# Kernel tuning notes

Measured on AMD Instinct MI355X. Metric: run time of the kernel, lower is better.

## Reference

```python
import jax, jax.numpy as jnp
import numpy as np

B, S, D, H = 1, 2048, 1280, 16
HD = D // H  # 80


def setup_inputs() -> dict:
    key = jax.random.key(0)
    ks = jax.random.split(key, 6)
    return {
        "hidden_states": jax.random.normal(ks[0], (B, S, D), dtype=jnp.float32),
        "rotary_pos_emb": jax.random.normal(ks[1], (S, HD // 2), dtype=jnp.float32),
        "qkv_w": jax.random.normal(ks[2], (3 * D, D), dtype=jnp.float32) * 0.02,
        "qkv_b": jax.random.normal(ks[3], (3 * D,), dtype=jnp.float32) * 0.02,
        "proj_w": jax.random.normal(ks[4], (D, D), dtype=jnp.float32) * 0.02,
        "proj_b": jax.random.normal(ks[5], (D,), dtype=jnp.float32) * 0.02,
    }


def reference(hidden_states, rotary_pos_emb, qkv_w, qkv_b, proj_w, proj_b):
    b, s, d = hidden_states.shape
    h = H
    hd = d // h
    scaling = hd ** -0.5

    # fused QKV projection: [b, s, 3*d]
    qkv = hidden_states @ qkv_w.T + qkv_b
    qkv = qkv.reshape(b, s, 3, h, hd)
    q, k, v = qkv[:, :, 0], qkv[:, :, 1], qkv[:, :, 2]  # each [b, s, h, hd]

    # rotary embedding: cos/sin [s, hd//2] -> [1, s, 1, hd]
    cos = jnp.cos(rotary_pos_emb)
    sin = jnp.sin(rotary_pos_emb)
    cos = jnp.concatenate([cos, cos], axis=-1)[None, :, None, :]
    sin = jnp.concatenate([sin, sin], axis=-1)[None, :, None, :]

    def apply_rope(x):
        x1, x2 = x[..., : hd // 2], x[..., hd // 2:]
        return x * cos + jnp.concatenate([-x2, x1], axis=-1) * sin

    q = apply_rope(q)
    k = apply_rope(k)

    # [b, h, s, hd]
    q = q.transpose(0, 2, 1, 3)
    k = k.transpose(0, 2, 1, 3)
    v = v.transpose(0, 2, 1, 3)

    # naive full attention matrix [b, h, s, s]
    attn = jnp.einsum("bhqd,bhkd->bhqk", q, k) * scaling
    attn = jax.nn.softmax(attn, axis=-1)
    out = jnp.einsum("bhqk,bhkd->bhqd", attn, v)
    out = out.transpose(0, 2, 1, 3).reshape(b, s, d)
    return out @ proj_w.T + proj_b
```

## Files before the change

### kernel.cpp

```cpp
#include <hip/hip_runtime.h>
#include <math.h>

#define SS 2048
#define DD 1280
#define HH 16
#define HDD 80
#define ND3 3840
#define ZZ 2

typedef __attribute__((ext_vector_type(8))) short short8;
typedef __attribute__((ext_vector_type(4))) short s16x4;
typedef __attribute__((ext_vector_type(4))) float f32x4;
typedef __attribute__((ext_vector_type(8))) _Float16 h16x8;
typedef __attribute__((ext_vector_type(4))) _Float16 h16x4;

__device__ inline short f2bf(float f) {
    union { float f; unsigned u; } x; x.f = f;
    unsigned r = x.u + 0x7FFF + ((x.u >> 16) & 1);
    return (short)(r >> 16);
}

__device__ inline void gload_lds16(const void* g, void* l) {
    __builtin_amdgcn_global_load_lds(
        (const __attribute__((address_space(1))) void*)g,
        (__attribute__((address_space(3))) void*)l, 16, 0, 0);
}

__global__ __launch_bounds__(256) void split_f16(
    const float* __restrict__ a, _Float16* __restrict__ ah, int nbA,
    const float* __restrict__ b, _Float16* __restrict__ bh, int nbB,
    const float* __restrict__ c, _Float16* __restrict__ ch)
{
    const float* x; _Float16* h;
    int blk = blockIdx.x;
    if (blk < nbA)            { x = a; h = ah; }
    else if (blk < nbA + nbB) { blk -= nbA; x = b; h = bh; }
    else                      { blk -= nbA + nbB; x = c; h = ch; }
    int i = (blk * 256 + threadIdx.x) * 4;
    float4 v = *(const float4*)(x + i);
    h16x4 hv;
    hv[0] = (_Float16)v.x; hv[1] = (_Float16)v.y;
    hv[2] = (_Float16)v.z; hv[3] = (_Float16)v.w;
    *(h16x4*)(h + i) = hv;
}

#define LDSA(m, kg) ((m) * 32 + (((kg) ^ (((m) >> 1) & 3)) << 3))

template <int BMT, int BNT>
__global__ __launch_bounds__(256) void gemm_f16(
    const _Float16* __restrict__ Ah, const _Float16* __restrict__ Bh,
    const float* __restrict__ bias, float* __restrict__ C,
    int M, int N, int K)
{
    constexpr int IT = BMT / 32;
    constexpr int JT = BNT / 32;
    constexpr int AU = BMT / 64;
    constexpr int BU = BNT / 64;
    __shared__ _Float16 AhS[2][BMT * 32];
    __shared__ _Float16 BhS[2][BNT * 32];

    const int tid = threadIdx.x;
    const int w = tid >> 6;
    const int lane = tid & 63;
    const int l15 = lane & 15;
    const int quad = lane >> 4;
    const int wm = w >> 1, wn = w & 1;
    const int bm = blockIdx.y * BMT;
    const int bn = blockIdx.x * BNT;

    f32x4 acc[IT][JT];
    #pragma unroll
    for (int i = 0; i < IT; ++i)
        #pragma unroll
        for (int j = 0; j < JT; ++j)
            acc[i][j] = (f32x4){0.f, 0.f, 0.f, 0.f};

    auto stage = [&](int buf, int k0) {
        #pragma unroll
        for (int u = 0; u < AU; ++u) {
            int i = tid + u * 256;
            int m = i >> 2;
            int kg = (i & 3) ^ ((m >> 1) & 3);
            gload_lds16(Ah + (size_t)(bm + m) * K + k0 + kg * 8,
                        &AhS[buf][(i & ~63) * 8]);
        }
        #pragma unroll
        for (int u = 0; u < BU; ++u) {
            int i = tid + u * 256;
            int m = i >> 2;
            int kg = (i & 3) ^ ((m >> 1) & 3);
            gload_lds16(Bh + (size_t)(bn + m) * K + k0 + kg * 8,
                        &BhS[buf][(i & ~63) * 8]);
        }
    };

    stage(0, 0);
    __syncthreads();
    int cur = 0;
    for (int k0 = 0; k0 < K; k0 += 32) {
        if (k0 + 32 < K) stage(cur ^ 1, k0 + 32);

        h16x8 af[IT], bf[JT];
        #pragma unroll
        for (int i = 0; i < IT; ++i) {
            int m = wm * (BMT / 2) + i * 16 + l15;
            af[i] = *(h16x8*)&AhS[cur][LDSA(m, quad)];
        }
        #pragma unroll
        for (int j = 0; j < JT; ++j) {
            int n = wn * (BNT / 2) + j * 16 + l15;
            bf[j] = *(h16x8*)&BhS[cur][LDSA(n, quad)];
        }
        #pragma unroll
        for (int i = 0; i < IT; ++i)
            #pragma unroll
            for (int j = 0; j < JT; ++j)
                acc[i][j] = __builtin_amdgcn_mfma_f32_16x16x32_f16(af[i], bf[j], acc[i][j], 0, 0, 0);

        __syncthreads();
        cur ^= 1;
    }

    #pragma unroll
    for (int j = 0; j < JT; ++j) {
        int col = bn + wn * (BNT / 2) + j * 16 + l15;
        float bb = bias[col];
        #pragma unroll
        for (int i = 0; i < IT; ++i)
            #pragma unroll
            for (int r = 0; r < 4; ++r) {
                int row = bm + wm * (BMT / 2) + i * 16 + quad * 4 + r;
                C[(size_t)row * N + col] = acc[i][j][r] + bb;
            }
    }
}

__global__ __launch_bounds__(256) void gemm_proj_merge(
    const _Float16* __restrict__ o_part, const float* __restrict__ l_part,
    const _Float16* __restrict__ Bh,
    const float* __restrict__ bias, float* __restrict__ C,
    int M, int N, int K)
{
    constexpr int BMT = 64, BNT = 128;
    constexpr int JT = BNT / 32;
    constexpr int BU = BNT / 64;
    __shared__ _Float16 AhS[BMT * 32];
    __shared__ _Float16 BhS[2][BNT * 32];
    __shared__ float linvS[HH * 64];

    const int tid = threadIdx.x;
    const int w = tid >> 6;
    const int lane = tid & 63;
    const int l15 = lane & 15;
    const int quad = lane >> 4;
    const int wm = w >> 1, wn = w & 1;
    const int bm = blockIdx.y * BMT;
    const int bn = blockIdx.x * BNT;

    for (int i = tid; i < HH * 64; i += 256) {
        int h = i >> 6, r = i & 63;
        float ls = 0.f;
        #pragma unroll
        for (int zi = 0; zi < ZZ; ++zi)
            ls += l_part[((size_t)zi * HH + h) * SS + bm + r];
        linvS[i] = 1.f / ls;
    }

    f32x4 acc[2][JT];
    #pragma unroll
    for (int i = 0; i < 2; ++i)
        #pragma unroll
        for (int j = 0; j < JT; ++j)
            acc[i][j] = (f32x4){0.f, 0.f, 0.f, 0.f};

    h16x8 ra[ZZ];
    auto loadgA = [&](int k0) {
        int m = tid >> 2, kg = tid & 3;
        size_t off = (size_t)(bm + m) * K + k0 + kg * 8;
        #pragma unroll
        for (int zi = 0; zi < ZZ; ++zi)
            ra[zi] = *(const h16x8*)(o_part + (size_t)zi * SS * DD + off);
    };
    auto stageB = [&](int buf, int k0) {
        #pragma unroll
        for (int u = 0; u < BU; ++u) {
            int i = tid + u * 256;
            int m = i >> 2;
            int kg = (i & 3) ^ ((m >> 1) & 3);
            gload_lds16(Bh + (size_t)(bn + m) * K + k0 + kg * 8,
                        &BhS[buf][(i & ~63) * 8]);
        }
    };

    stageB(0, 0);
    loadgA(0);
    __syncthreads();
    int cur = 0;
    for (int k0 = 0; k0 < K; k0 += 32) {
        {
            int m = tid >> 2, kg = tid & 3;
            int koff = k0 + kg * 8;
            int h = koff / HDD;
            float inv = linvS[h * 64 + m];
            h16x8 f;
            #pragma unroll
            for (int e = 0; e < 8; ++e) {
                float s = (float)ra[0][e];
                #pragma unroll
                for (int zi = 1; zi < ZZ; ++zi) s += (float)ra[zi][e];
                f[e] = (_Float16)(s * inv);
            }
            *(h16x8*)&AhS[LDSA(m, kg)] = f;
        }
        __syncthreads();

        if (k0 + 32 < K) {
            stageB(cur ^ 1, k0 + 32);
            loadgA(k0 + 32);
        }

        h16x8 af[2], bf[JT];
        #pragma unroll
        for (int i = 0; i < 2; ++i) {
            int m = wm * 32 + i * 16 + l15;
            af[i] = *(h16x8*)&AhS[LDSA(m, quad)];
        }
        #pragma unroll
        for (int j = 0; j < JT; ++j) {
            int n = wn * 64 + j * 16 + l15;
            bf[j] = *(h16x8*)&BhS[cur][LDSA(n, quad)];
        }
        #pragma unroll
        for (int i = 0; i < 2; ++i)
            #pragma unroll
            for (int j = 0; j < JT; ++j)
                acc[i][j] = __builtin_amdgcn_mfma_f32_16x16x32_f16(af[i], bf[j], acc[i][j], 0, 0, 0);

        __syncthreads();
        cur ^= 1;
    }

    #pragma unroll
    for (int j = 0; j < JT; ++j) {
        int col = bn + wn * 64 + j * 16 + l15;
        float bb = bias[col];
        #pragma unroll
        for (int i = 0; i < 2; ++i)
            #pragma unroll
            for (int r = 0; r < 4; ++r) {
                int row = bm + wm * 32 + i * 16 + quad * 4 + r;
                C[(size_t)row * N + col] = acc[i][j][r] + bb;
            }
    }
}

__global__ __launch_bounds__(256) void rope_scatter_bf16(
    const float* __restrict__ qkv, const float* __restrict__ rpe,
    short* __restrict__ q, short* __restrict__ k, short* __restrict__ v)
{
    __shared__ __align__(16) float cs[40], sn[40];
    const int s = blockIdx.x;
    if (threadIdx.x < 40)
        __sincosf(rpe[s * 40 + threadIdx.x], &sn[threadIdx.x], &cs[threadIdx.x]);
    __syncthreads();
    const float scale = 0.11180339887498949f;
    const float* src = qkv + (size_t)s * ND3;
    for (int t = threadIdx.x; t < ND3 / 4; t += 256) {
        int j4 = t * 4;
        int p = j4 / DD;
        int rem = j4 - p * DD;
        int hh = rem / HDD;
        int d = rem - hh * HDD;
        float4 x = *(const float4*)(src + j4);
        float vv[4];
        if (p == 2) {
            vv[0] = x.x; vv[1] = x.y; vv[2] = x.z; vv[3] = x.w;
        } else {
            bool lo = d < 40;
            int dm = lo ? d : d - 40;
            float4 oth = *(const float4*)(src + p * DD + hh * HDD + (lo ? d + 40 : d - 40));
            float4 c4 = *(const float4*)&cs[dm];
            float4 s4 = *(const float4*)&sn[dm];
            float sg = lo ? -1.f : 1.f;
            vv[0] = x.x * c4.x + sg * oth.x * s4.x;
            vv[1] = x.y * c4.y + sg * oth.y * s4.y;
            vv[2] = x.z * c4.z + sg * oth.z * s4.z;
            vv[3] = x.w * c4.w + sg * oth.w * s4.w;
            if (p == 0) { vv[0] *= scale; vv[1] *= scale; vv[2] *= scale; vv[3] *= scale; }
        }
        short* dst = (p == 0) ? q : (p == 1) ? k : v;
        s16x4 o4;
        o4[0] = f2bf(vv[0]); o4[1] = f2bf(vv[1]);
        o4[2] = f2bf(vv[2]); o4[3] = f2bf(vv[3]);
        *(s16x4*)(dst + ((size_t)hh * SS + s) * HDD + d) = o4;
    }
}

__global__ __launch_bounds__(512, 4) void attn_mfma(
    const short* __restrict__ q, const short* __restrict__ k,
    const short* __restrict__ v, _Float16* __restrict__ o_part,
    float* __restrict__ l_part)
{
    __shared__ short Ks[64][104];
    __shared__ short Vts[80 * 64];
    __shared__ short Ps[8][16 * 64];

    const int h = blockIdx.y;
    const int q0 = blockIdx.x << 7;
    const int z = blockIdx.z;
    const int tid = threadIdx.x;
    const int w = tid >> 6;
    const int lane = tid & 63;
    const int l15 = lane & 15;
    const int quad = lane >> 4;

    const short* qbase = q + (size_t)h * SS * HDD;
    const short* kbase = k + (size_t)h * SS * HDD;
    const short* vbase = v + (size_t)h * SS * HDD;

    short8 qf[3];
    {
        const int row = q0 + w * 16 + l15;
        #pragma unroll
        for (int kk = 0; kk < 3; ++kk) {
            int c0 = kk * 32 + quad * 8;
            qf[kk] = (c0 < HDD) ? *(const short8*)(qbase + (size_t)row * HDD + c0)
                                : (short8)0;
        }
    }

    if (tid < 128) {
        int r = tid >> 1, c = 80 + (tid & 1) * 8;
        *(short8*)&Ks[r][c] = (short8)0;
    }

    float lsum[4] = {0.f, 0.f, 0.f, 0.f};
    f32x4 o[5];
    #pragma unroll
    for (int n = 0; n < 5; ++n) o[n] = (f32x4){0.f, 0.f, 0.f, 0.f};

    const int kt0 = z << 10;
    for (int kt = kt0; kt < kt0 + 1024; kt += 64) {
        __syncthreads();
        #pragma unroll
        for (int u = 0; u < 2; ++u) {
            int i = tid + u * 512;
            if (i < 640) {
                int r = i / 10, c = (i - r * 10) * 8;
                *(short8*)&Ks[r][c] = *(const short8*)(kbase + (size_t)(kt + r) * HDD + c);
            }
        }
        {
            int task = tid;
            if (task < 320) {
                int r4 = (task & 15) << 2;
                int d4 = (task >> 4) << 2;
                s16x4 a0 = *(const s16x4*)(vbase + (size_t)(kt + r4 + 0) * HDD + d4);
                s16x4 a1 = *(const s16x4*)(vbase + (size_t)(kt + r4 + 1) * HDD + d4);
                s16x4 a2 = *(const s16x4*)(vbase + (size_t)(kt + r4 + 2) * HDD + d4);
                s16x4 a3 = *(const s16x4*)(vbase + (size_t)(kt + r4 + 3) * HDD + d4);
                #pragma unroll
                for (int j = 0; j < 4; ++j) {
                    s16x4 w4 = {a0[j], a1[j], a2[j], a3[j]};
                    int d = d4 + j;
                    int sw = (r4 >> 3) ^ (d & 7);
                    *(s16x4*)&Vts[d * 64 + sw * 8 + (r4 & 7)] = w4;
                }
            }
        }
        __syncthreads();

        f32x4 s_[4];
        #pragma unroll
        for (int nt = 0; nt < 4; ++nt) {
            short8 bf0 = *(short8*)&Ks[nt * 16 + l15][quad * 8];
            short8 bf1 = *(short8*)&Ks[nt * 16 + l15][32 + quad * 8];
            short8 bf2 = *(short8*)&Ks[nt * 16 + l15][64 + quad * 8];
            f32x4 acc = (f32x4){0.f, 0.f, 0.f, 0.f};
            acc = __builtin_amdgcn_mfma_f32_16x16x32_bf16(qf[0], bf0, acc, 0, 0, 0);
            acc = __builtin_amdgcn_mfma_f32_16x16x32_bf16(qf[1], bf1, acc, 0, 0, 0);
            acc = __builtin_amdgcn_mfma_f32_16x16x32_bf16(qf[2], bf2, acc, 0, 0, 0);
            s_[nt] = acc;
        }

        #pragma unroll
        for (int nt = 0; nt < 4; ++nt)
            #pragma unroll
            for (int r = 0; r < 4; ++r) {
                float p = __expf(s_[nt][r] - 8.f);
                lsum[r] += p;
                int row = quad * 4 + r;
                int g = (nt * 2 + (l15 >> 3)) ^ (row & 7);
                Ps[w][row * 64 + g * 8 + (l15 & 7)] = f2bf(p);
            }

        short8 pf[2];
        #pragma unroll
        for (int kk = 0; kk < 2; ++kk) {
            int g = (kk * 4 + quad) ^ (l15 & 7);
            pf[kk] = *(short8*)&Ps[w][l15 * 64 + g * 8];
        }
        #pragma unroll
        for (int n = 0; n < 5; ++n) {
            #pragma unroll
            for (int kk = 0; kk < 2; ++kk) {
                int d = n * 16 + l15;
                int sw = (kk * 4 + quad) ^ (l15 & 7);
                short8 vf = *(short8*)&Vts[d * 64 + sw * 8];
                o[n] = __builtin_amdgcn_mfma_f32_16x16x32_bf16(pf[kk], vf, o[n], 0, 0, 0);
            }
        }
    }

    _Float16* ob = o_part + (size_t)z * SS * DD;
    #pragma unroll
    for (int r = 0; r < 4; ++r) {
        float rs = lsum[r];
        #pragma unroll
        for (int off = 1; off < 16; off <<= 1)
            rs += __shfl_xor(rs, off, 64);
        lsum[r] = rs;
    }
    #pragma unroll
    for (int n = 0; n < 5; ++n)
        #pragma unroll
        for (int r = 0; r < 4; ++r) {
            int row = q0 + w * 16 + quad * 4 + r;
            ob[(size_t)row * DD + h * HDD + n * 16 + l15] = (_Float16)o[n][r];
        }
    if (l15 == 0)
        #pragma unroll
        for (int r = 0; r < 4; ++r)
            l_part[((size_t)z * HH + h) * SS + q0 + w * 16 + quad * 4 + r] = lsum[r];
}

extern "C" void kernel_launch(void* const* d_in, const int* in_sizes, int n_in,
                              void* d_out, int out_size, void* d_ws, size_t ws_size,
                              hipStream_t stream)
{
    const float* hs     = (const float*)d_in[0];
    const float* rpe    = (const float*)d_in[1];
    const float* qkv_w  = (const float*)d_in[2];
    const float* qkv_b  = (const float*)d_in[3];
    const float* proj_w = (const float*)d_in[4];
    const float* proj_b = (const float*)d_in[5];
    float* out = (float*)d_out;

    short* s0 = (short*)d_ws;
    float* qkv_f  = (float*)d_ws;
    _Float16* o_part = (_Float16*)s0;
    float* l_part = (float*)(s0 + 10485760);
    short* s1 = s0 + 15728640;
    _Float16* qkvw_h = (_Float16*)s1;
    short* qb = s1;
    short* kb = s1 + 2621440;
    short* vb = s1 + 5242880;
    short* s2 = s1 + 7864320;
    _Float16* hs_h = (_Float16*)s2;
    short* s3 = s2 + 2621440;
    _Float16* projw_h = (_Float16*)s3;

    const int n_hs = SS * DD;
    const int n_qw = ND3 * DD;
    const int n_pw = DD * DD;

    split_f16<<<n_hs / 1024 + n_qw / 1024 + n_pw / 1024, 256, 0, stream>>>(
        hs, hs_h, n_hs / 1024,
        qkv_w, qkvw_h, n_qw / 1024,
        proj_w, projw_h);
    gemm_f16<128, 128><<<dim3(ND3 / 128, SS / 128), 256, 0, stream>>>(
        hs_h, qkvw_h, qkv_b, qkv_f, SS, ND3, DD);
    rope_scatter_bf16<<<SS, 256, 0, stream>>>(qkv_f, rpe, qb, kb, vb);
    attn_mfma<<<dim3(SS / 128, HH, ZZ), 512, 0, stream>>>(qb, kb, vb, o_part, l_part);
    gemm_proj_merge<<<dim3(DD / 128, SS / 64), 256, 0, stream>>>(
        o_part, l_part, projw_h, proj_b, out, SS, DD, DD);
}
```

Baseline: 211.2 us.

## Double-buffer K/V tiles with register prefetch in attention kernel

The attention kernel now loads the next K/V tile from global memory into registers before computing on the current tile, then writes it into a second LDS buffer after the MFMAs. This overlaps global load latency with compute and cuts the loop to one barrier per iteration. s_setprio is also raised around the MFMA sections. LDS use roughly doubles for K/V, which may reduce occupancy under launch_bounds(512,4), and the extra prefetch registers add register pressure.

```diff
diff --git a/kernel.cpp b/kernel.cpp
--- a/kernel.cpp
+++ b/kernel.cpp
@@ -301,8 +301,8 @@
     const short* __restrict__ v, _Float16* __restrict__ o_part,
     float* __restrict__ l_part)
 {
-    __shared__ short Ks[64][104];
-    __shared__ short Vts[80 * 64];
+    __shared__ short Ks[2][64][104];
+    __shared__ short Vts[2][80 * 64];
     __shared__ short Ps[8][16 * 64];
 
     const int h = blockIdx.y;
@@ -329,9 +329,11 @@
         }
     }
 
-    if (tid < 128) {
-        int r = tid >> 1, c = 80 + (tid & 1) * 8;
-        *(short8*)&Ks[r][c] = (short8)0;
+    if (tid < 256) {
+        int b = tid >> 7;
+        int t2 = tid & 127;
+        int r = t2 >> 1, c = 80 + (t2 & 1) * 8;
+        *(short8*)&Ks[b][r][c] = (short8)0;
     }
 
     float lsum[4] = {0.f, 0.f, 0.f, 0.f};
@@ -339,49 +341,69 @@
     #pragma unroll
     for (int n = 0; n < 5; ++n) o[n] = (f32x4){0.f, 0.f, 0.f, 0.f};
 
-    const int kt0 = z << 10;
-    for (int kt = kt0; kt < kt0 + 1024; kt += 64) {
-        __syncthreads();
+    short8 kr[2];
+    s16x4 vr[4];
+    auto issueKV = [&](int kt) {
         #pragma unroll
         for (int u = 0; u < 2; ++u) {
             int i = tid + u * 512;
             if (i < 640) {
                 int r = i / 10, c = (i - r * 10) * 8;
-                *(short8*)&Ks[r][c] = *(const short8*)(kbase + (size_t)(kt + r) * HDD + c);
-            }
-        }
-        {
-            int task = tid;
-            if (task < 320) {
-                int r4 = (task & 15) << 2;
-                int d4 = (task >> 4) << 2;
-                s16x4 a0 = *(const s16x4*)(vbase + (size_t)(kt + r4 + 0) * HDD + d4);
-                s16x4 a1 = *(const s16x4*)(vbase + (size_t)(kt + r4 + 1) * HDD + d4);
-                s16x4 a2 = *(const s16x4*)(vbase + (size_t)(kt + r4 + 2) * HDD + d4);
-                s16x4 a3 = *(const s16x4*)(vbase + (size_t)(kt + r4 + 3) * HDD + d4);
-                #pragma unroll
-                for (int j = 0; j < 4; ++j) {
-                    s16x4 w4 = {a0[j], a1[j], a2[j], a3[j]};
-                    int d = d4 + j;
-                    int sw = (r4 >> 3) ^ (d & 7);
-                    *(s16x4*)&Vts[d * 64 + sw * 8 + (r4 & 7)] = w4;
-                }
-            }
-        }
-        __syncthreads();
+                kr[u] = *(const short8*)(kbase + (size_t)(kt + r) * HDD + c);
+            }
+        }
+        if (tid < 320) {
+            int r4 = (tid & 15) << 2, d4 = (tid >> 4) << 2;
+            #pragma unroll
+            for (int j = 0; j < 4; ++j)
+                vr[j] = *(const s16x4*)(vbase + (size_t)(kt + r4 + j) * HDD + d4);
+        }
+    };
+    auto writeKV = [&](int buf) {
+        #pragma unroll
+        for (int u = 0; u < 2; ++u) {
+            int i = tid + u * 512;
+            if (i < 640) {
+                int r = i / 10, c = (i - r * 10) * 8;
+                *(short8*)&Ks[buf][r][c] = kr[u];
+            }
+        }
+        if (tid < 320) {
+            int r4 = (tid & 15) << 2, d4 = (tid >> 4) << 2;
+            #pragma unroll
+            for (int j = 0; j < 4; ++j) {
+                s16x4 w4 = {vr[0][j], vr[1][j], vr[2][j], vr[3][j]};
+                int d = d4 + j;
+                int sw = (r4 >> 3) ^ (d & 7);
+                *(s16x4*)&Vts[buf][d * 64 + sw * 8 + (r4 & 7)] = w4;
+            }
+        }
+    };
+
+    const int kt0 = z << 10;
+    issueKV(kt0);
+    writeKV(0);
+    __syncthreads();
+    int cur = 0;
+    for (int t = 0; t < 16; ++t) {
+        const int kt = kt0 + t * 64;
+        const bool more = (t + 1 < 16);
+        if (more) issueKV(kt + 64);
 
         f32x4 s_[4];
+        __builtin_amdgcn_s_setprio(1);
         #pragma unroll
         for (int nt = 0; nt < 4; ++nt) {
-            short8 bf0 = *(short8*)&Ks[nt * 16 + l15][quad * 8];
-            short8 bf1 = *(short8*)&Ks[nt * 16 + l15][32 + quad * 8];
-            short8 bf2 = *(short8*)&Ks[nt * 16 + l15][64 + quad * 8];
+            short8 bf0 = *(short8*)&Ks[cur][nt * 16 + l15][quad * 8];
+            short8 bf1 = *(short8*)&Ks[cur][nt * 16 + l15][32 + quad * 8];
+            short8 bf2 = *(short8*)&Ks[cur][nt * 16 + l15][64 + quad * 8];
             f32x4 acc = (f32x4){0.f, 0.f, 0.f, 0.f};
             acc = __builtin_amdgcn_mfma_f32_16x16x32_bf16(qf[0], bf0, acc, 0, 0, 0);
             acc = __builtin_amdgcn_mfma_f32_16x16x32_bf16(qf[1], bf1, acc, 0, 0, 0);
             acc = __builtin_amdgcn_mfma_f32_16x16x32_bf16(qf[2], bf2, acc, 0, 0, 0);
             s_[nt] = acc;
         }
+        __builtin_amdgcn_s_setprio(0);
 
         #pragma unroll
         for (int nt = 0; nt < 4; ++nt)
@@ -400,16 +422,22 @@
             int g = (kk * 4 + quad) ^ (l15 & 7);
             pf[kk] = *(short8*)&Ps[w][l15 * 64 + g * 8];
         }
+        __builtin_amdgcn_s_setprio(1);
         #pragma unroll
         for (int n = 0; n < 5; ++n) {
             #pragma unroll
             for (int kk = 0; kk < 2; ++kk) {
                 int d = n * 16 + l15;
                 int sw = (kk * 4 + quad) ^ (l15 & 7);
-                short8 vf = *(short8*)&Vts[d * 64 + sw * 8];
+                short8 vf = *(short8*)&Vts[cur][d * 64 + sw * 8];
                 o[n] = __builtin_amdgcn_mfma_f32_16x16x32_bf16(pf[kk], vf, o[n], 0, 0, 0);
             }
         }
+        __builtin_amdgcn_s_setprio(0);
+
+        if (more) writeKV(cur ^ 1);
+        __syncthreads();
+        cur ^= 1;
     }
 
     _Float16* ob = o_part + (size_t)z * SS * DD;
```

Result: faster. 206.5 us (-2.2%).
